# Kernel tuning notes

Hardware: AMD Instinct MI355X
Metric: run time of the kernel (lower is better)

Reference implementation:

```python
import jax, jax.numpy as jnp
import numpy as np

N, E = 50000, 800000
IN_DIM, H, D = 128, 8, 16  # num_heads=8, out_dim(per head)=16


def setup_inputs() -> dict:
    key = jax.random.key(0)
    ks = jax.random.split(key, 9)
    s = 1.0 / np.sqrt(IN_DIM)
    return {
        "h": jax.random.normal(ks[0], (N, IN_DIM), dtype=jnp.float32),
        "Wq": jax.random.normal(ks[1], (IN_DIM, H * D), dtype=jnp.float32) * s,
        "bq": jnp.zeros((H * D,), dtype=jnp.float32),
        "Wk": jax.random.normal(ks[2], (IN_DIM, H * D), dtype=jnp.float32) * s,
        "bk": jnp.zeros((H * D,), dtype=jnp.float32),
        "Wv": jax.random.normal(ks[3], (IN_DIM, H * D), dtype=jnp.float32) * s,
        "bv": jnp.zeros((H * D,), dtype=jnp.float32),
        "src": jax.random.randint(ks[4], (E,), 0, N, dtype=jnp.int32),
        "dst": jax.random.randint(ks[5], (E,), 0, N, dtype=jnp.int32),
    }


def reference(h, Wq, bq, Wk, bk, Wv, bv, src, dst):
    n = h.shape[0]
    Q = (h @ Wq + bq).reshape(n, H, D)
    K = (h @ Wk + bk).reshape(n, H, D)
    V = (h @ Wv + bv).reshape(n, H, D)
    # edge score: u_mul_v(K, Q).sum(-1) / sqrt(D), clamped to [-5, 5]
    score = jnp.einsum("ehd,ehd->eh", K[src], Q[dst]) / jnp.sqrt(
        jnp.asarray(D, h.dtype)
    )  # [E, H]
    score = jnp.clip(score, -5.0, 5.0)
    # edge_softmax over edges sharing the same destination node
    smax = jax.ops.segment_max(score, dst, num_segments=n)  # [N, H]
    ex = jnp.exp(score - smax[dst])
    denom = jax.ops.segment_sum(ex, dst, num_segments=n)  # [N, H]
    a = ex / denom[dst]  # [E, H]
    # u_mul_e(V, a) then sum to destination
    m = V[src] * a[:, :, None]  # [E, H, D]
    wV = jax.ops.segment_sum(m, dst, num_segments=n)  # [N, H, D]
    return wV.reshape(n, H * D)
```

## Files before the change

kernel.cpp:

```cpp
#include <hip/hip_runtime.h>
#include <hip/hip_bf16.h>


typedef short short8 __attribute__((ext_vector_type(8)));
typedef float f32x4 __attribute__((ext_vector_type(4)));

__device__ __forceinline__ unsigned pack_bf16(float a, float b) {
    unsigned ua = __float_as_uint(a), ub = __float_as_uint(b);
    ua += 0x7fffu + ((ua >> 16) & 1u);
    ub += 0x7fffu + ((ub >> 16) & 1u);
    return (ua >> 16) | (ub & 0xffff0000u);
}

#define ULO(u) __uint_as_float((u) << 16)
#define UHI(u) __uint_as_float((u) & 0xffff0000u)

__global__ __launch_bounds__(256) void prep_all(
    const float* __restrict__ W0, const float* __restrict__ W1,
    const float* __restrict__ W2, const float* __restrict__ h,
    unsigned char* __restrict__ WTb, unsigned char* __restrict__ hb,
    int* __restrict__ counts, int n, int hB)
{
    const int b = blockIdx.x;
    if (b < 24) {
        const int w   = b >> 3;
        const int idx = (b & 7) * 256 + threadIdx.x;
        const float* W = (w == 0) ? W0 : (w == 1) ? W1 : W2;
        unsigned char* wt = WTb + w * 32768;
        const int kp = idx >> 5;
        const int c4 = (idx & 31) * 4;
        const float* Wp = W + (size_t)(2 * kp) * 128 + c4;
        float4 wa = *(const float4*)Wp;
        float4 wb = *(const float4*)(Wp + 128);
        float a0[4] = {wa.x, wa.y, wa.z, wa.w};
        float a1[4] = {wb.x, wb.y, wb.z, wb.w};
#pragma unroll
        for (int i = 0; i < 4; ++i) {
            const int col = c4 + i;
            *(unsigned*)(wt + col * 256 + ((4 * kp) ^ ((col & 7) << 4))) =
                pack_bf16(a0[i], a1[i]);
        }
    } else if (b < 24 + hB) {
        const int idx = (b - 24) * 256 + threadIdx.x;
        const int row = idx >> 5;
        const int c4  = (idx & 31) * 4;
        float4 v = make_float4(0.f, 0.f, 0.f, 0.f);
        if (row < n) v = *(const float4*)(h + (size_t)row * 128 + c4);
        *(uint2*)(hb + row * 256 + ((c4 * 2) ^ ((row & 7) << 4))) =
            make_uint2(pack_bf16(v.x, v.y), pack_bf16(v.z, v.w));
    } else {
        const int i = (b - 24 - hB) * 256 + threadIdx.x;
        if (i < n) counts[i] = 0;
    }
}

__global__ void hist_rank(const int* __restrict__ dst, int* __restrict__ counts,
                          int* __restrict__ rank, int e) {
    int i = blockIdx.x * blockDim.x + threadIdx.x;
    if (i < e) rank[i] = atomicAdd(&counts[dst[i]], 1);
}

__global__ void scan_block_sums(const int* __restrict__ counts, int* __restrict__ bsums, int nelem) {
    __shared__ int red[4];
    int i = blockIdx.x * 256 + threadIdx.x;
    int v = (i < nelem) ? counts[i] : 0;
#pragma unroll
    for (int o = 32; o > 0; o >>= 1) v += __shfl_down(v, o, 64);
    if ((threadIdx.x & 63) == 0) red[threadIdx.x >> 6] = v;
    __syncthreads();
    if (threadIdx.x == 0) bsums[blockIdx.x] = red[0] + red[1] + red[2] + red[3];
}

__global__ void scan_final2(const int* __restrict__ counts, const int* __restrict__ bsums,
                            int* __restrict__ offsets, int nelem, int e) {
    __shared__ int tmp[256];
    __shared__ int red[4];
    const int t = threadIdx.x;

    int pre = (t < blockIdx.x) ? bsums[t] : 0;
#pragma unroll
    for (int o = 32; o > 0; o >>= 1) pre += __shfl_down(pre, o, 64);
    if ((t & 63) == 0) red[t >> 6] = pre;
    __syncthreads();
    const int base = red[0] + red[1] + red[2] + red[3];

    const int i = blockIdx.x * 256 + t;
    int v = (i < nelem) ? counts[i] : 0;
    tmp[t] = v;
    __syncthreads();
    for (int o = 1; o < 256; o <<= 1) {
        int u = (t >= o) ? tmp[t - o] : 0;
        __syncthreads();
        tmp[t] += u;
        __syncthreads();
    }
    if (i < nelem) offsets[i] = base + tmp[t] - v;
    if (i == nelem) offsets[nelem] = e;
}

__global__ void fill_kernel(const int* __restrict__ src, const int* __restrict__ dst,
                            const int* __restrict__ rank, const int* __restrict__ offsets,
                            int* __restrict__ srcSorted, int e) {
    int i = blockIdx.x * blockDim.x + threadIdx.x;
    if (i < e) srcSorted[offsets[dst[i]] + rank[i]] = src[i];
}

__global__ __launch_bounds__(512) void qkv_gemm_mfma(
    const unsigned char* __restrict__ hb, const unsigned char* __restrict__ WTb,
    const float* __restrict__ b0, const float* __restrict__ b1,
    const float* __restrict__ b2,
    unsigned* __restrict__ qb, unsigned* __restrict__ kb, unsigned* __restrict__ vb)
{
    __shared__ __align__(16) unsigned char lds[49152];
    const int tid  = threadIdx.x;
    const int row0 = blockIdx.x * 64;

    {
        const uint4* s = (const uint4*)(hb + (size_t)row0 * 256);
        uint4* d = (uint4*)lds;
        d[tid]       = s[tid];
        d[tid + 512] = s[tid + 512];
    }

    const float* bs[3] = {b0, b1, b2};
    unsigned* planes[3] = {qb, kb, vb};

    const int lane = tid & 63, wave = tid >> 6;
    const int wr = wave >> 2, wc = wave & 3;
    const int lr = lane & 15, lg = lane >> 4;

    for (int w = 0; w < 3; ++w) {
        __syncthreads();
        {
            const uint4* s = (const uint4*)(WTb + w * 32768);
            uint4* d = (uint4*)(lds + 16384);
#pragma unroll
            for (int t = 0; t < 4; ++t) d[tid + t * 512] = s[tid + t * 512];
        }
        __syncthreads();

        f32x4 acc[2][2];
#pragma unroll
        for (int nt = 0; nt < 2; ++nt) {
            const float bv = bs[w][wc * 32 + nt * 16 + lr];
            acc[0][nt] = (f32x4){bv, bv, bv, bv};
            acc[1][nt] = (f32x4){bv, bv, bv, bv};
        }
#pragma unroll
        for (int ks = 0; ks < 4; ++ks) {
            const int kbyte = ks * 64 + lg * 16;
            short8 af[2], bf[2];
#pragma unroll
            for (int mt = 0; mt < 2; ++mt) {
                const int row = wr * 32 + mt * 16 + lr;
                af[mt] = *(const short8*)(lds + row * 256 + (kbyte ^ ((row & 7) << 4)));
            }
#pragma unroll
            for (int nt = 0; nt < 2; ++nt) {
                const int col = wc * 32 + nt * 16 + lr;
                bf[nt] = *(const short8*)(lds + 16384 + col * 256 + (kbyte ^ ((col & 7) << 4)));
            }
#pragma unroll
            for (int mt = 0; mt < 2; ++mt)
#pragma unroll
                for (int nt = 0; nt < 2; ++nt)
                    acc[mt][nt] = __builtin_amdgcn_mfma_f32_16x16x32_bf16(
                        af[mt], bf[nt], acc[mt][nt], 0, 0, 0);
        }

        __syncthreads();
        {
            unsigned* epi = (unsigned*)(lds + 16384);
#pragma unroll
            for (int mt = 0; mt < 2; ++mt)
#pragma unroll
                for (int nt = 0; nt < 2; ++nt) {
                    const int col = wc * 32 + nt * 16 + lr;
#pragma unroll
                    for (int r = 0; r < 4; ++r) {
                        const int row = wr * 32 + mt * 16 + lg * 4 + r;
                        const float v  = acc[mt][nt][r];
                        const float vn = __shfl_xor(v, 1);
                        if (!(lane & 1)) epi[row * 64 + (col >> 1)] = pack_bf16(v, vn);
                    }
                }
        }
        __syncthreads();
        {
            const uint4* s = (const uint4*)(lds + 16384);
            uint4* d = (uint4*)(planes[w] + (size_t)row0 * 64);
            d[tid]       = s[tid];
            d[tid + 512] = s[tid + 512];
        }
    }
}

__global__ __launch_bounds__(256) void mha_node(
    const unsigned* __restrict__ Qb, const unsigned* __restrict__ Kb,
    const unsigned* __restrict__ Vb,
    const int* __restrict__ offsets, const int* __restrict__ srcSorted,
    float* __restrict__ out, int n)
{
    const int lane = threadIdx.x & 63;
    const int node = (blockIdx.x * blockDim.x + threadIdx.x) >> 6;
    if (node >= n) return;

    const unsigned qu = Qb[(size_t)node * 64 + lane];
    const float qx = ULO(qu) * 0.25f, qy = UHI(qu) * 0.25f;
    const int beg = offsets[node], end = offsets[node + 1];

    float accx = 0.f, accy = 0.f, lsum = 0.f;

#define EDGE_COMPUTE(ku, vu)                                          \
    {                                                                 \
        float prod = fmaf(ULO(ku), qx, UHI(ku) * qy);                 \
        prod += __shfl_xor(prod, 1);                                  \
        prod += __shfl_xor(prod, 2);                                  \
        prod += __shfl_xor(prod, 4);                                  \
        float sc = fminf(5.f, fmaxf(-5.f, prod));                     \
        float p = __expf(sc);                                         \
        lsum += p;                                                    \
        accx = fmaf(p, ULO(vu), accx);                                \
        accy = fmaf(p, UHI(vu), accy);                                \
    }

    for (int j0 = beg; j0 < end; j0 += 64) {
        const int rem = end - j0;
        const int cnt = rem < 64 ? rem : 64;
        int myS = (lane < cnt) ? srcSorted[j0 + lane] : 0;

        int t = 0;
        for (; t + 8 <= cnt; t += 8) {
            unsigned ku[8], vu[8];
#pragma unroll
            for (int u = 0; u < 8; ++u) {
                int s = __shfl(myS, t + u);
                ku[u] = Kb[(size_t)s * 64 + lane];
                vu[u] = Vb[(size_t)s * 64 + lane];
            }
#pragma unroll
            for (int u = 0; u < 8; ++u) EDGE_COMPUTE(ku[u], vu[u]);
        }
        for (; t < cnt; ++t) {
            int s = __shfl(myS, t);
            unsigned ku0 = Kb[(size_t)s * 64 + lane];
            unsigned vu0 = Vb[(size_t)s * 64 + lane];
            EDGE_COMPUTE(ku0, vu0);
        }
    }

    float inv = (lsum > 0.f) ? 1.f / lsum : 0.f;
    *(float2*)(out + (size_t)node * 128 + lane * 2) =
        make_float2(accx * inv, accy * inv);
}

extern "C" void kernel_launch(void* const* d_in, const int* in_sizes, int n_in,
                              void* d_out, int out_size, void* d_ws, size_t ws_size,
                              hipStream_t stream) {
    const float* h  = (const float*)d_in[0];
    const float* Wq = (const float*)d_in[1];
    const float* bq = (const float*)d_in[2];
    const float* Wk = (const float*)d_in[3];
    const float* bk = (const float*)d_in[4];
    const float* Wv = (const float*)d_in[5];
    const float* bv = (const float*)d_in[6];
    const int*   src = (const int*)d_in[7];
    const int*   dst = (const int*)d_in[8];
    float* out = (float*)d_out;

    const int n = in_sizes[0] / 128;
    const int e = in_sizes[7];
    const int nblk = (n + 63) / 64;
    const int npad = nblk * 64;
    const int nb = (n + 255) / 256;
    const int hB = npad / 8;
    const int zB = nb;

    char* ws = (char*)d_ws;
    size_t off = 0;
    auto alloc = [&](size_t bytes) {
        char* p = ws + off;
        off = (off + bytes + 255) & ~(size_t)255;
        return p;
    };
    unsigned char* hb  = (unsigned char*)alloc((size_t)npad * 256);
    unsigned char* WTb = (unsigned char*)alloc(3 * 32768);
    unsigned* Qb       = (unsigned*)alloc((size_t)npad * 64 * 4);
    unsigned* Kb       = (unsigned*)alloc((size_t)npad * 64 * 4);
    unsigned* Vb       = (unsigned*)alloc((size_t)npad * 64 * 4);
    int* counts        = (int*)alloc((size_t)n * sizeof(int));
    int* offsets       = (int*)alloc((size_t)(n + 1) * sizeof(int));
    int* rank          = (int*)alloc((size_t)e * sizeof(int));
    int* bsums         = (int*)alloc((size_t)nb * sizeof(int));
    int* srcSorted     = (int*)alloc((size_t)e * sizeof(int));
    (void)ws_size; (void)n_in; (void)out_size;

    prep_all<<<24 + hB + zB, 256, 0, stream>>>(Wq, Wk, Wv, h, WTb, hb, counts, n, hB);
    hist_rank<<<(e + 255) / 256, 256, 0, stream>>>(dst, counts, rank, e);
    scan_block_sums<<<nb, 256, 0, stream>>>(counts, bsums, n);
    scan_final2<<<nb, 256, 0, stream>>>(counts, bsums, offsets, n, e);
    fill_kernel<<<(e + 255) / 256, 256, 0, stream>>>(src, dst, rank, offsets, srcSorted, e);
    qkv_gemm_mfma<<<nblk, 512, 0, stream>>>(hb, WTb, bq, bk, bv, Qb, Kb, Vb);
    mha_node<<<((size_t)n * 64 + 255) / 256, 256, 0, stream>>>(
        Qb, Kb, Vb, offsets, srcSorted, out, n);
}
```

Measured before the change: 147.4 us.

## Replace two-pass scan with decoupled lookback and fuse CSR fill into GEMM

The two scan kernels become a single-pass scan with decoupled lookback, using a per-block state array that prep_all zeroes. The CSR fill loop now runs as a grid-stride loop at the start of the QKV GEMM kernel, and the mha_node edge loop gathers 16 edges at a time before computing. Together this removes two kernel launches and exposes more memory-level parallelism in the gather. The lookback depends on earlier blocks making progress, and the 16-wide unroll raises register pressure.

```diff
diff --git a/kernel.cpp b/kernel.cpp
--- a/kernel.cpp
+++ b/kernel.cpp
@@ -19,7 +19,8 @@
     const float* __restrict__ W0, const float* __restrict__ W1,
     const float* __restrict__ W2, const float* __restrict__ h,
     unsigned char* __restrict__ WTb, unsigned char* __restrict__ hb,
-    int* __restrict__ counts, int n, int hB)
+    int* __restrict__ counts, unsigned long long* __restrict__ state,
+    int n, int hB, int nbS)
 {
     const int b = blockIdx.x;
     if (b < 24) {
@@ -49,8 +50,10 @@
         *(uint2*)(hb + row * 256 + ((c4 * 2) ^ ((row & 7) << 4))) =
             make_uint2(pack_bf16(v.x, v.y), pack_bf16(v.z, v.w));
     } else {
-        const int i = (b - 24 - hB) * 256 + threadIdx.x;
+        const int zb = b - 24 - hB;
+        const int i = zb * 256 + threadIdx.x;
         if (i < n) counts[i] = 0;
+        if (zb == 0 && threadIdx.x < nbS) state[threadIdx.x] = 0ull;
     }
 }
 
@@ -60,31 +63,15 @@
     if (i < e) rank[i] = atomicAdd(&counts[dst[i]], 1);
 }
 
-__global__ void scan_block_sums(const int* __restrict__ counts, int* __restrict__ bsums, int nelem) {
-    __shared__ int red[4];
-    int i = blockIdx.x * 256 + threadIdx.x;
-    int v = (i < nelem) ? counts[i] : 0;
-#pragma unroll
-    for (int o = 32; o > 0; o >>= 1) v += __shfl_down(v, o, 64);
-    if ((threadIdx.x & 63) == 0) red[threadIdx.x >> 6] = v;
-    __syncthreads();
-    if (threadIdx.x == 0) bsums[blockIdx.x] = red[0] + red[1] + red[2] + red[3];
-}
-
-__global__ void scan_final2(const int* __restrict__ counts, const int* __restrict__ bsums,
-                            int* __restrict__ offsets, int nelem, int e) {
+__global__ __launch_bounds__(256) void scan_onepass(
+    const int* __restrict__ counts, unsigned long long* __restrict__ state,
+    int* __restrict__ offsets, int nelem, int e)
+{
     __shared__ int tmp[256];
-    __shared__ int red[4];
-    const int t = threadIdx.x;
-
-    int pre = (t < blockIdx.x) ? bsums[t] : 0;
-#pragma unroll
-    for (int o = 32; o > 0; o >>= 1) pre += __shfl_down(pre, o, 64);
-    if ((t & 63) == 0) red[t >> 6] = pre;
-    __syncthreads();
-    const int base = red[0] + red[1] + red[2] + red[3];
-
-    const int i = blockIdx.x * 256 + t;
+    __shared__ int sbase;
+    const int t = threadIdx.x, b = blockIdx.x;
+    const int i = b * 256 + t;
+
     int v = (i < nelem) ? counts[i] : 0;
     tmp[t] = v;
     __syncthreads();
@@ -94,27 +81,54 @@
         tmp[t] += u;
         __syncthreads();
     }
+    const int agg = tmp[255];
+
+    if (t == 0) {
+        if (b == 0) {
+            __hip_atomic_store(&state[0],
+                ((unsigned long long)(unsigned)agg << 32) | 2ull,
+                __ATOMIC_RELEASE, __HIP_MEMORY_SCOPE_AGENT);
+            sbase = 0;
+        } else {
+            __hip_atomic_store(&state[b],
+                ((unsigned long long)(unsigned)agg << 32) | 1ull,
+                __ATOMIC_RELEASE, __HIP_MEMORY_SCOPE_AGENT);
+            int run = 0, j = b - 1;
+            while (true) {
+                unsigned long long s = __hip_atomic_load(&state[j],
+                    __ATOMIC_ACQUIRE, __HIP_MEMORY_SCOPE_AGENT);
+                unsigned f = (unsigned)(s & 3ull);
+                if (f == 2u) { run += (int)(s >> 32); break; }
+                if (f == 1u) { run += (int)(s >> 32); --j; }
+            }
+            __hip_atomic_store(&state[b],
+                ((unsigned long long)(unsigned)(run + agg) << 32) | 2ull,
+                __ATOMIC_RELEASE, __HIP_MEMORY_SCOPE_AGENT);
+            sbase = run;
+        }
+    }
+    __syncthreads();
+    const int base = sbase;
     if (i < nelem) offsets[i] = base + tmp[t] - v;
     if (i == nelem) offsets[nelem] = e;
 }
 
-__global__ void fill_kernel(const int* __restrict__ src, const int* __restrict__ dst,
-                            const int* __restrict__ rank, const int* __restrict__ offsets,
-                            int* __restrict__ srcSorted, int e) {
-    int i = blockIdx.x * blockDim.x + threadIdx.x;
-    if (i < e) srcSorted[offsets[dst[i]] + rank[i]] = src[i];
-}
-
-__global__ __launch_bounds__(512) void qkv_gemm_mfma(
+__global__ __launch_bounds__(512) void gemm_fill(
     const unsigned char* __restrict__ hb, const unsigned char* __restrict__ WTb,
     const float* __restrict__ b0, const float* __restrict__ b1,
     const float* __restrict__ b2,
-    unsigned* __restrict__ qb, unsigned* __restrict__ kb, unsigned* __restrict__ vb)
+    unsigned* __restrict__ qb, unsigned* __restrict__ kb, unsigned* __restrict__ vb,
+    const int* __restrict__ src, const int* __restrict__ dst,
+    const int* __restrict__ rank, const int* __restrict__ offsets,
+    int* __restrict__ srcSorted, int e)
 {
     __shared__ __align__(16) unsigned char lds[49152];
-    const int tid  = threadIdx.x;
+    const int tid = threadIdx.x;
+
+    for (int i = blockIdx.x * 512 + tid; i < e; i += gridDim.x * 512)
+        srcSorted[offsets[dst[i]] + rank[i]] = src[i];
+
     const int row0 = blockIdx.x * 64;
-
     {
         const uint4* s = (const uint4*)(hb + (size_t)row0 * 256);
         uint4* d = (uint4*)lds;
@@ -230,7 +244,18 @@
         int myS = (lane < cnt) ? srcSorted[j0 + lane] : 0;
 
         int t = 0;
-        for (; t + 8 <= cnt; t += 8) {
+        for (; t + 16 <= cnt; t += 16) {
+            unsigned ku[16], vu[16];
+#pragma unroll
+            for (int u = 0; u < 16; ++u) {
+                int s = __shfl(myS, t + u);
+                ku[u] = Kb[(size_t)s * 64 + lane];
+                vu[u] = Vb[(size_t)s * 64 + lane];
+            }
+#pragma unroll
+            for (int u = 0; u < 16; ++u) EDGE_COMPUTE(ku[u], vu[u]);
+        }
+        if (t + 8 <= cnt) {
             unsigned ku[8], vu[8];
 #pragma unroll
             for (int u = 0; u < 8; ++u) {
@@ -240,6 +265,7 @@
             }
 #pragma unroll
             for (int u = 0; u < 8; ++u) EDGE_COMPUTE(ku[u], vu[u]);
+            t += 8;
         }
         for (; t < cnt; ++t) {
             int s = __shfl(myS, t);
@@ -291,16 +317,16 @@
     int* counts        = (int*)alloc((size_t)n * sizeof(int));
     int* offsets       = (int*)alloc((size_t)(n + 1) * sizeof(int));
     int* rank          = (int*)alloc((size_t)e * sizeof(int));
-    int* bsums         = (int*)alloc((size_t)nb * sizeof(int));
+    unsigned long long* state = (unsigned long long*)alloc((size_t)nb * 8);
     int* srcSorted     = (int*)alloc((size_t)e * sizeof(int));
     (void)ws_size; (void)n_in; (void)out_size;
 
-    prep_all<<<24 + hB + zB, 256, 0, stream>>>(Wq, Wk, Wv, h, WTb, hb, counts, n, hB);
+    prep_all<<<24 + hB + zB, 256, 0, stream>>>(Wq, Wk, Wv, h, WTb, hb,
+                                               counts, state, n, hB, nb);
     hist_rank<<<(e + 255) / 256, 256, 0, stream>>>(dst, counts, rank, e);
-    scan_block_sums<<<nb, 256, 0, stream>>>(counts, bsums, n);
-    scan_final2<<<nb, 256, 0, stream>>>(counts, bsums, offsets, n, e);
-    fill_kernel<<<(e + 255) / 256, 256, 0, stream>>>(src, dst, rank, offsets, srcSorted, e);
-    qkv_gemm_mfma<<<nblk, 512, 0, stream>>>(hb, WTb, bq, bk, bv, Qb, Kb, Vb);
+    scan_onepass<<<nb, 256, 0, stream>>>(counts, state, offsets, n, e);
+    gemm_fill<<<nblk, 512, 0, stream>>>(hb, WTb, bq, bk, bv, Qb, Kb, Vb,
+                                        src, dst, rank, offsets, srcSorted, e);
     mha_node<<<((size_t)n * 64 + 255) / 256, 256, 0, stream>>>(
         Qb, Kb, Vb, offsets, srcSorted, out, n);
 }
```

After: 177.5 us. +20.5%, slower.

## Fuse h bf16 conversion into QKV GEMM and read weights directly from global

Applied to the files above, without the earlier changes.

Removes the separate h-to-bf16 conversion pass in prep_all and the hb workspace buffer. The GEMM kernel now loads fp32 h directly, converts and swizzles it into LDS, and preloads the A fragments into registers once. Weight fragments are read straight from global memory (L2-resident) instead of being staged through LDS, which drops the per-weight syncthreads. This saves a full write and read of the bf16 h copy, but adds register pressure and relies on cache hits for the uncoalesced weight fragment loads.

```diff
diff --git a/kernel.cpp b/kernel.cpp
--- a/kernel.cpp
+++ b/kernel.cpp
@@ -17,9 +17,8 @@
 
 __global__ __launch_bounds__(256) void prep_all(
     const float* __restrict__ W0, const float* __restrict__ W1,
-    const float* __restrict__ W2, const float* __restrict__ h,
-    unsigned char* __restrict__ WTb, unsigned char* __restrict__ hb,
-    int* __restrict__ counts, int n, int hB)
+    const float* __restrict__ W2, unsigned char* __restrict__ WTb,
+    int* __restrict__ counts, int n)
 {
     const int b = blockIdx.x;
     if (b < 24) {
@@ -40,16 +39,8 @@
             *(unsigned*)(wt + col * 256 + ((4 * kp) ^ ((col & 7) << 4))) =
                 pack_bf16(a0[i], a1[i]);
         }
-    } else if (b < 24 + hB) {
-        const int idx = (b - 24) * 256 + threadIdx.x;
-        const int row = idx >> 5;
-        const int c4  = (idx & 31) * 4;
-        float4 v = make_float4(0.f, 0.f, 0.f, 0.f);
-        if (row < n) v = *(const float4*)(h + (size_t)row * 128 + c4);
-        *(uint2*)(hb + row * 256 + ((c4 * 2) ^ ((row & 7) << 4))) =
-            make_uint2(pack_bf16(v.x, v.y), pack_bf16(v.z, v.w));
     } else {
-        const int i = (b - 24 - hB) * 256 + threadIdx.x;
+        const int i = (b - 24) * 256 + threadIdx.x;
         if (i < n) counts[i] = 0;
     }
 }
@@ -105,21 +96,24 @@
     if (i < e) srcSorted[offsets[dst[i]] + rank[i]] = src[i];
 }
 
-__global__ __launch_bounds__(512) void qkv_gemm_mfma(
-    const unsigned char* __restrict__ hb, const unsigned char* __restrict__ WTb,
+__global__ __launch_bounds__(512) void qkv_gemm(
+    const float* __restrict__ h, const unsigned char* __restrict__ WTb,
     const float* __restrict__ b0, const float* __restrict__ b1,
     const float* __restrict__ b2,
-    unsigned* __restrict__ qb, unsigned* __restrict__ kb, unsigned* __restrict__ vb)
+    unsigned* __restrict__ qb, unsigned* __restrict__ kb, unsigned* __restrict__ vb,
+    int n)
 {
-    __shared__ __align__(16) unsigned char lds[49152];
+    __shared__ __align__(16) unsigned char lds[32768];
     const int tid  = threadIdx.x;
     const int row0 = blockIdx.x * 64;
 
-    {
-        const uint4* s = (const uint4*)(hb + (size_t)row0 * 256);
-        uint4* d = (uint4*)lds;
-        d[tid]       = s[tid];
-        d[tid + 512] = s[tid + 512];
+    for (int idx = tid; idx < 2048; idx += 512) {
+        const int row = idx >> 5;
+        const int c4  = (idx & 31) * 4;
+        float4 v = make_float4(0.f, 0.f, 0.f, 0.f);
+        if (row0 + row < n) v = *(const float4*)(h + (size_t)(row0 + row) * 128 + c4);
+        *(uint2*)(lds + row * 256 + ((c4 * 2) ^ ((row & 7) << 4))) =
+            make_uint2(pack_bf16(v.x, v.y), pack_bf16(v.z, v.w));
     }
 
     const float* bs[3] = {b0, b1, b2};
@@ -129,15 +123,29 @@
     const int wr = wave >> 2, wc = wave & 3;
     const int lr = lane & 15, lg = lane >> 4;
 
+    __syncthreads();
+
+    short8 af[2][4];
+#pragma unroll
+    for (int mt = 0; mt < 2; ++mt)
+#pragma unroll
+        for (int ks = 0; ks < 4; ++ks) {
+            const int row = wr * 32 + mt * 16 + lr;
+            const int kbyte = ks * 64 + lg * 16;
+            af[mt][ks] = *(const short8*)(lds + row * 256 + (kbyte ^ ((row & 7) << 4)));
+        }
+
     for (int w = 0; w < 3; ++w) {
-        __syncthreads();
-        {
-            const uint4* s = (const uint4*)(WTb + w * 32768);
-            uint4* d = (uint4*)(lds + 16384);
-#pragma unroll
-            for (int t = 0; t < 4; ++t) d[tid + t * 512] = s[tid + t * 512];
-        }
-        __syncthreads();
+        short8 bf[2][4];
+#pragma unroll
+        for (int nt = 0; nt < 2; ++nt)
+#pragma unroll
+            for (int ks = 0; ks < 4; ++ks) {
+                const int col = wc * 32 + nt * 16 + lr;
+                const int kbyte = ks * 64 + lg * 16;
+                bf[nt][ks] = *(const short8*)(
+                    WTb + w * 32768 + col * 256 + (kbyte ^ ((col & 7) << 4)));
+            }
 
         f32x4 acc[2][2];
 #pragma unroll
@@ -147,26 +155,13 @@
             acc[1][nt] = (f32x4){bv, bv, bv, bv};
         }
 #pragma unroll
-        for (int ks = 0; ks < 4; ++ks) {
-            const int kbyte = ks * 64 + lg * 16;
-            short8 af[2], bf[2];
-#pragma unroll
-            for (int mt = 0; mt < 2; ++mt) {
-                const int row = wr * 32 + mt * 16 + lr;
-                af[mt] = *(const short8*)(lds + row * 256 + (kbyte ^ ((row & 7) << 4)));
-            }
-#pragma unroll
-            for (int nt = 0; nt < 2; ++nt) {
-                const int col = wc * 32 + nt * 16 + lr;
-                bf[nt] = *(const short8*)(lds + 16384 + col * 256 + (kbyte ^ ((col & 7) << 4)));
-            }
+        for (int ks = 0; ks < 4; ++ks)
 #pragma unroll
             for (int mt = 0; mt < 2; ++mt)
 #pragma unroll
                 for (int nt = 0; nt < 2; ++nt)
                     acc[mt][nt] = __builtin_amdgcn_mfma_f32_16x16x32_bf16(
-                        af[mt], bf[nt], acc[mt][nt], 0, 0, 0);
-        }
+                        af[mt][ks], bf[nt][ks], acc[mt][nt], 0, 0, 0);
 
         __syncthreads();
         {
@@ -273,8 +268,6 @@
     const int nblk = (n + 63) / 64;
     const int npad = nblk * 64;
     const int nb = (n + 255) / 256;
-    const int hB = npad / 8;
-    const int zB = nb;
 
     char* ws = (char*)d_ws;
     size_t off = 0;
@@ -283,7 +276,6 @@
         off = (off + bytes + 255) & ~(size_t)255;
         return p;
     };
-    unsigned char* hb  = (unsigned char*)alloc((size_t)npad * 256);
     unsigned char* WTb = (unsigned char*)alloc(3 * 32768);
     unsigned* Qb       = (unsigned*)alloc((size_t)npad * 64 * 4);
     unsigned* Kb       = (unsigned*)alloc((size_t)npad * 64 * 4);
@@ -295,12 +287,12 @@
     int* srcSorted     = (int*)alloc((size_t)e * sizeof(int));
     (void)ws_size; (void)n_in; (void)out_size;
 
-    prep_all<<<24 + hB + zB, 256, 0, stream>>>(Wq, Wk, Wv, h, WTb, hb, counts, n, hB);
+    prep_all<<<24 + nb, 256, 0, stream>>>(Wq, Wk, Wv, WTb, counts, n);
     hist_rank<<<(e + 255) / 256, 256, 0, stream>>>(dst, counts, rank, e);
     scan_block_sums<<<nb, 256, 0, stream>>>(counts, bsums, n);
     scan_final2<<<nb, 256, 0, stream>>>(counts, bsums, offsets, n, e);
     fill_kernel<<<(e + 255) / 256, 256, 0, stream>>>(src, dst, rank, offsets, srcSorted, e);
-    qkv_gemm_mfma<<<nblk, 512, 0, stream>>>(hb, WTb, bq, bk, bv, Qb, Kb, Vb);
+    qkv_gemm<<<nblk, 512, 0, stream>>>(h, WTb, bq, bk, bv, Qb, Kb, Vb, n);
     mha_node<<<((size_t)n * 64 + 255) / 256, 256, 0, stream>>>(
         Qb, Kb, Vb, offsets, srcSorted, out, n);
 }
```

Result: faster. 143.7 us (-2.5%).
